# Kernel optimization log

Measured on AMD Instinct MI355X. Metric: run time of the kernel, lower is better.

## Reference

```python
import jax, jax.numpy as jnp
import numpy as np

DIM = 768
HEADS = 12
DIM_HEAD = DIM // HEADS
FACTOR = DIM_HEAD ** (-0.5)
B, T = 4, 2048


def setup_inputs() -> dict:
    key = jax.random.key(0)
    k1, k2, k3 = jax.random.split(key, 3)
    x = jax.random.normal(k1, (B, T, DIM), dtype=jnp.float32)
    # VarianceScaling-like init scale for linear weights
    W_qkv = jax.random.normal(k2, (DIM, 3 * DIM), dtype=jnp.float32) * (DIM ** -0.5)
    W_out = jax.random.normal(k3, (DIM, DIM), dtype=jnp.float32) * (DIM ** -0.5)
    return {"x": x, "W_qkv": W_qkv, "W_out": W_out}


def reference(x, W_qkv, W_out):
    b, t, _ = x.shape
    qkv = x @ W_qkv  # [b, t, 3*dim]
    # einops 'b t (d k h) -> k b h t d' with k=3, h=HEADS: d slowest, k middle, h fastest
    qkv = qkv.reshape(b, t, DIM_HEAD, 3, HEADS)
    qkv = jnp.transpose(qkv, (3, 0, 4, 1, 2))  # [3, b, h, t, d]
    q, k, v = qkv[0], qkv[1], qkv[2]
    # scaled dot-product attention, full [b,h,t,t] scores as in the original
    scores = jnp.einsum('bhid,bhjd->bhij', q, k) * FACTOR
    attn = jax.nn.softmax(scores, axis=-1)
    out = jnp.einsum('bhij,bhjd->bhid', attn, v)  # [b, h, t, d]
    # 'b h t d -> b t (h d)'
    out = jnp.transpose(out, (0, 2, 1, 3)).reshape(b, t, HEADS * DIM_HEAD)
    return out @ W_out
```

## Files before the change

kernel.cpp:

```cpp
#include <hip/hip_runtime.h>
#include <hip/hip_bf16.h>

#define DIM    768
#define HEADS  12
#define DHEAD  64
#define BATCH  4
#define SEQ    2048
#define NROW   (BATCH * SEQ)
#define QKVN   (3 * DIM)
#define FACTOR 0.125f

typedef __attribute__((ext_vector_type(8))) short short8;
typedef __attribute__((ext_vector_type(4))) float floatx4;

__device__ __forceinline__ floatx4 mfma16(short8 a, short8 b, floatx4 c) {
    return __builtin_amdgcn_mfma_f32_16x16x32_bf16(a, b, c, 0, 0, 0);
}

__device__ __forceinline__ short f2b(float f) {
    union { __hip_bfloat16 h; short s; } u;
    u.h = __float2bfloat16(f);
    return u.s;
}

__device__ __forceinline__ int swz8(int row, int col) {
    return (row << 6) + ((((col >> 3) ^ row) & 7) << 3) + (col & 7);
}

__global__ __launch_bounds__(256) void conv_bf16(const float* __restrict__ x,
                                                 short* __restrict__ xb) {
    int g = blockIdx.x * 256 + threadIdx.x;
    float4 v = ((const float4*)x)[g];
    uint2 o;
    o.x = (unsigned short)f2b(v.x) | ((unsigned)(unsigned short)f2b(v.y) << 16);
    o.y = (unsigned short)f2b(v.z) | ((unsigned)(unsigned short)f2b(v.w) << 16);
    ((uint2*)xb)[g] = o;
}

__global__ __launch_bounds__(256) void transpose_w(const float* __restrict__ W,
                                                   short* __restrict__ Wt,
                                                   int K, int N, int permute) {
    __shared__ short T[32][33];
    int n0 = blockIdx.x * 32, k0 = blockIdx.y * 32;
    int c = threadIdx.x & 31, r0 = threadIdx.x >> 5;
    for (int r = r0; r < 32; r += 8)
        T[r][c] = f2b(W[(size_t)(k0 + r) * N + n0 + c]);
    __syncthreads();
    for (int r = r0; r < 32; r += 8) {
        int n = n0 + r;
        int np;
        if (permute) {
            int d = n / 36, rem = n - d * 36;
            int which = rem / 12, h = rem - which * 12;
            np = which * 768 + h * 64 + d;
        } else {
            np = n;
        }
        Wt[(size_t)np * K + k0 + c] = T[c][r];
    }
}

__global__ __launch_bounds__(256) void gemm_qkv(const short* __restrict__ A,
                                                const short* __restrict__ Bt,
                                                short* __restrict__ Qo,
                                                short* __restrict__ Ko,
                                                short* __restrict__ Vto) {
    __shared__ short As[128 * 64];
    __shared__ short Bs[128 * 64];
    const int tid = threadIdx.x;
    const int lane = tid & 63, wave = tid >> 6;
    const int l15 = lane & 15, quad = lane >> 4;

    const int flat = blockIdx.x;
    const int xcd = flat & 7;
    const int local = flat >> 3;
    const int mloc = local & 7, nloc = local >> 3;
    const int m0 = (xcd * 8 + mloc) * 128;
    const int n0 = nloc * 128;

    const int wm = (wave >> 1) * 64, wn = (wave & 1) * 64;

    floatx4 acc[4][4] = {};
    for (int k0 = 0; k0 < DIM; k0 += 64) {
#pragma unroll
        for (int i = 0; i < 4; ++i) {
            int idx = tid + i * 256;
            int row = idx >> 3, c = idx & 7;
            int loff = (row << 6) + (((c ^ row) & 7) << 3);
            *(uint4*)&As[loff] = *(const uint4*)&A[(size_t)(m0 + row) * DIM + k0 + c * 8];
            *(uint4*)&Bs[loff] = *(const uint4*)&Bt[(size_t)(n0 + row) * DIM + k0 + c * 8];
        }
        __syncthreads();
#pragma unroll
        for (int ks = 0; ks < 2; ++ks) {
            short8 a[4], b[4];
#pragma unroll
            for (int mt = 0; mt < 4; ++mt)
                a[mt] = *(const short8*)&As[swz8(wm + mt * 16 + l15, ks * 32 + quad * 8)];
#pragma unroll
            for (int nt = 0; nt < 4; ++nt)
                b[nt] = *(const short8*)&Bs[swz8(wn + nt * 16 + l15, ks * 32 + quad * 8)];
#pragma unroll
            for (int mt = 0; mt < 4; ++mt)
#pragma unroll
                for (int nt = 0; nt < 4; ++nt)
                    acc[mt][nt] = mfma16(a[mt], b[nt], acc[mt][nt]);
        }
        __syncthreads();
    }

    const int sn = n0 + wn;
    const int which = sn / 768;
    const int h = (sn - which * 768) >> 6;
    const int bb = (m0 + wm) >> 11;
    const int tbase = (m0 + wm) & 2047;

    if (which != 2) {
        short* dst = (which == 0) ? Qo : Ko;
        const size_t rowbase = ((size_t)(bb * HEADS + h) * SEQ + tbase) * DHEAD;
#pragma unroll
        for (int mt = 0; mt < 4; ++mt)
#pragma unroll
            for (int nt = 0; nt < 4; ++nt) {
                int d = nt * 16 + l15;
#pragma unroll
                for (int r = 0; r < 4; ++r) {
                    int tl = mt * 16 + quad * 4 + r;
                    dst[rowbase + (size_t)tl * DHEAD + d] = f2b(acc[mt][nt][r]);
                }
            }
    } else {
        short* vld = ((wave < 2) ? As : Bs) + (wave & 1) * 4096;
#pragma unroll
        for (int mt = 0; mt < 4; ++mt)
#pragma unroll
            for (int nt = 0; nt < 4; ++nt) {
                int d = nt * 16 + l15;
                int tl = mt * 16 + quad * 4;
                int chunk = (tl >> 3) ^ (d & 7);
                int addr = (d << 6) + (chunk << 3) + (tl & 7);
                short4 pk;
                pk.x = f2b(acc[mt][nt][0]);
                pk.y = f2b(acc[mt][nt][1]);
                pk.z = f2b(acc[mt][nt][2]);
                pk.w = f2b(acc[mt][nt][3]);
                *(short4*)&vld[addr] = pk;
            }
    }
    __syncthreads();
    if (which == 2) {
        short* vld = ((wave < 2) ? As : Bs) + (wave & 1) * 4096;
        const size_t vbase = ((size_t)(bb * HEADS + h) * DHEAD) * SEQ;
#pragma unroll
        for (int i = 0; i < 8; ++i) {
            int c = lane + i * 64;
            int d = c >> 3, j = c & 7;
            int addr = (d << 6) + (((j ^ (d & 7)) & 7) << 3);
            uint4 v = *(const uint4*)&vld[addr];
            *(uint4*)&Vto[vbase + (size_t)d * SEQ + tbase + j * 8] = v;
        }
    }
}

__global__ __launch_bounds__(256) void attn_mfma(const short* __restrict__ Q,
                                                 const short* __restrict__ K,
                                                 const short* __restrict__ Vt,
                                                 short* __restrict__ O) {
    __shared__ short Qs[128 * 64];
    __shared__ short Ks[64 * 64];
    __shared__ short Vs[64 * 64];
    __shared__ short Ps[4 * 32 * 64];

    const int tid = threadIdx.x;
    const int lane = tid & 63, wave = tid >> 6;
    const int l15 = lane & 15, quad = lane >> 4;
    const int bh = blockIdx.y;
    const int q0 = blockIdx.x * 128;
    const size_t base = (size_t)bh * SEQ * DHEAD;
    const int wr = wave * 32;
    short* myP = Ps + wave * (32 * 64);
    const float LOG2E_F = 1.4426950408889634f * FACTOR;

#pragma unroll
    for (int i = 0; i < 4; ++i) {
        int idx = tid + i * 256;
        int row = idx >> 3, c = idx & 7;
        *(uint4*)&Qs[(row << 6) + (((c ^ row) & 7) << 3)] =
            *(const uint4*)&Q[base + (size_t)(q0 + row) * DHEAD + c * 8];
    }

    floatx4 o[2][4] = {};
    float lsum[2][4] = {};

    for (int j0 = 0; j0 < SEQ; j0 += 64) {
#pragma unroll
        for (int i = 0; i < 2; ++i) {
            int idx = tid + i * 256;
            int row = idx >> 3, c = idx & 7;
            int loff = (row << 6) + (((c ^ row) & 7) << 3);
            *(uint4*)&Ks[loff] = *(const uint4*)&K[base + (size_t)(j0 + row) * DHEAD + c * 8];
            *(uint4*)&Vs[loff] = *(const uint4*)&Vt[base + (size_t)row * SEQ + j0 + c * 8];
        }
        __syncthreads();

        floatx4 s[2][4] = {};
#pragma unroll
        for (int ks = 0; ks < 2; ++ks) {
            short8 a[2], b[4];
#pragma unroll
            for (int mt = 0; mt < 2; ++mt)
                a[mt] = *(const short8*)&Qs[swz8(wr + mt * 16 + l15, ks * 32 + quad * 8)];
#pragma unroll
            for (int nt = 0; nt < 4; ++nt)
                b[nt] = *(const short8*)&Ks[swz8(nt * 16 + l15, ks * 32 + quad * 8)];
#pragma unroll
            for (int mt = 0; mt < 2; ++mt)
#pragma unroll
                for (int nt = 0; nt < 4; ++nt)
                    s[mt][nt] = mfma16(a[mt], b[nt], s[mt][nt]);
        }

#pragma unroll
        for (int mt = 0; mt < 2; ++mt)
#pragma unroll
            for (int r = 0; r < 4; ++r) {
                int lrow = mt * 16 + quad * 4 + r;
                float rs = 0.f;
#pragma unroll
                for (int nt = 0; nt < 4; ++nt) {
                    float p = __builtin_amdgcn_exp2f(s[mt][nt][r] * LOG2E_F);
                    rs += p;
                    myP[swz8(lrow, nt * 16 + l15)] = f2b(p);
                }
                lsum[mt][r] += rs;
            }

#pragma unroll
        for (int ks = 0; ks < 2; ++ks) {
            short8 a[2], b[4];
#pragma unroll
            for (int mt = 0; mt < 2; ++mt)
                a[mt] = *(const short8*)&myP[swz8(mt * 16 + l15, ks * 32 + quad * 8)];
#pragma unroll
            for (int dt = 0; dt < 4; ++dt)
                b[dt] = *(const short8*)&Vs[swz8(dt * 16 + l15, ks * 32 + quad * 8)];
#pragma unroll
            for (int mt = 0; mt < 2; ++mt)
#pragma unroll
                for (int dt = 0; dt < 4; ++dt)
                    o[mt][dt] = mfma16(a[mt], b[dt], o[mt][dt]);
        }
        __syncthreads();
    }

    const int b = bh / HEADS, h = bh - b * HEADS;
#pragma unroll
    for (int mt = 0; mt < 2; ++mt)
#pragma unroll
        for (int r = 0; r < 4; ++r) {
            float rs = lsum[mt][r];
#pragma unroll
            for (int off = 1; off < 16; off <<= 1) rs += __shfl_xor(rs, off);
            float inv = 1.f / rs;
            int t = q0 + wr + mt * 16 + quad * 4 + r;
#pragma unroll
            for (int dt = 0; dt < 4; ++dt) {
                int d = dt * 16 + l15;
                O[((size_t)(b * SEQ + t)) * DIM + h * DHEAD + d] =
                    f2b(o[mt][dt][r] * inv);
            }
        }
}

__global__ __launch_bounds__(256) void gemm_out(const short* __restrict__ A,
                                                const short* __restrict__ Bt,
                                                float* __restrict__ out) {
    __shared__ short As[128 * 64];
    __shared__ short Bs[128 * 64];
    const int tid = threadIdx.x;
    const int lane = tid & 63, wave = tid >> 6;
    const int l15 = lane & 15, quad = lane >> 4;
    const int m0 = blockIdx.y * 128, n0 = blockIdx.x * 128;
    const int wm = (wave >> 1) * 64, wn = (wave & 1) * 64;

    floatx4 acc[4][4] = {};
    for (int k0 = 0; k0 < DIM; k0 += 64) {
#pragma unroll
        for (int i = 0; i < 4; ++i) {
            int idx = tid + i * 256;
            int row = idx >> 3, c = idx & 7;
            int loff = (row << 6) + (((c ^ row) & 7) << 3);
            *(uint4*)&As[loff] = *(const uint4*)&A[(size_t)(m0 + row) * DIM + k0 + c * 8];
            *(uint4*)&Bs[loff] = *(const uint4*)&Bt[(size_t)(n0 + row) * DIM + k0 + c * 8];
        }
        __syncthreads();
#pragma unroll
        for (int ks = 0; ks < 2; ++ks) {
            short8 a[4], b[4];
#pragma unroll
            for (int mt = 0; mt < 4; ++mt)
                a[mt] = *(const short8*)&As[swz8(wm + mt * 16 + l15, ks * 32 + quad * 8)];
#pragma unroll
            for (int nt = 0; nt < 4; ++nt)
                b[nt] = *(const short8*)&Bs[swz8(wn + nt * 16 + l15, ks * 32 + quad * 8)];
#pragma unroll
            for (int mt = 0; mt < 4; ++mt)
#pragma unroll
                for (int nt = 0; nt < 4; ++nt)
                    acc[mt][nt] = mfma16(a[mt], b[nt], acc[mt][nt]);
        }
        __syncthreads();
    }

#pragma unroll
    for (int mt = 0; mt < 4; ++mt)
#pragma unroll
        for (int nt = 0; nt < 4; ++nt)
#pragma unroll
            for (int r = 0; r < 4; ++r) {
                int m = m0 + wm + mt * 16 + quad * 4 + r;
                int n = n0 + wn + nt * 16 + l15;
                out[(size_t)m * DIM + n] = acc[mt][nt][r];
            }
}

extern "C" void kernel_launch(void* const* d_in, const int* in_sizes, int n_in,
                              void* d_out, int out_size, void* d_ws, size_t ws_size,
                              hipStream_t stream) {
    const float* x    = (const float*)d_in[0];
    const float* Wqkv = (const float*)d_in[1];
    const float* Wout = (const float*)d_in[2];
    float* out = (float*)d_out;

    const size_t NE = (size_t)NROW * DIM;
    short* xb  = (short*)d_ws;
    short* Wqt = xb + NE;
    short* Wot = Wqt + (size_t)QKVN * DIM;
    short* Qw  = Wot + (size_t)DIM * DIM;
    short* Kw  = Qw + NE;
    short* Vtw = Kw + NE;

    conv_bf16<<<NE / 4 / 256, 256, 0, stream>>>(x, xb);
    transpose_w<<<dim3(QKVN / 32, DIM / 32), 256, 0, stream>>>(Wqkv, Wqt, DIM, QKVN, 1);
    transpose_w<<<dim3(DIM / 32, DIM / 32), 256, 0, stream>>>(Wout, Wot, DIM, DIM, 0);
    gemm_qkv<<<8 * 8 * 18, 256, 0, stream>>>(xb, Wqt, Qw, Kw, Vtw);
    attn_mfma<<<dim3(SEQ / 128, BATCH * HEADS), 256, 0, stream>>>(Qw, Kw, Vtw, xb);
    gemm_out<<<dim3(DIM / 128, NROW / 128), 256, 0, stream>>>(xb, Wot, out);
}
```

Before: 253.9 us.

## Fold softmax scale into Q and compute transposed scores for packed P stores

Folds the softmax factor times log2(e) into Q when the QKV GEMM writes it out, so the attention loop applies exp2 directly without a per-element multiply. It also swaps the MFMA operands so each lane holds four consecutive keys of one query row, which lets P be packed two at a time into 64-bit LDS stores and the row sums be reduced with two shuffles instead of four. The generic bf16 conversion is replaced by a hand-written round-to-nearest-even bit trick with pairwise packing. Scaling Q before rounding to bf16 changes rounding slightly, and the no-max softmax still depends on the scores staying small.

```diff
diff --git a/kernel.cpp b/kernel.cpp
--- a/kernel.cpp
+++ b/kernel.cpp
@@ -9,6 +9,7 @@
 #define NROW   (BATCH * SEQ)
 #define QKVN   (3 * DIM)
 #define FACTOR 0.125f
+#define QSCALE 0.18033688011112042f
 
 typedef __attribute__((ext_vector_type(8))) short short8;
 typedef __attribute__((ext_vector_type(4))) float floatx4;
@@ -17,10 +18,16 @@
     return __builtin_amdgcn_mfma_f32_16x16x32_bf16(a, b, c, 0, 0, 0);
 }
 
-__device__ __forceinline__ short f2b(float f) {
-    union { __hip_bfloat16 h; short s; } u;
-    u.h = __float2bfloat16(f);
-    return u.s;
+__device__ __forceinline__ short rne16(float f) {
+    unsigned u = __builtin_bit_cast(unsigned, f);
+    return (short)((u + 0x7fffu + ((u >> 16) & 1u)) >> 16);
+}
+__device__ __forceinline__ unsigned pack2(float lo, float hi) {
+    unsigned ul = __builtin_bit_cast(unsigned, lo);
+    unsigned uh = __builtin_bit_cast(unsigned, hi);
+    ul = (ul + 0x7fffu + ((ul >> 16) & 1u)) >> 16;
+    uh = (uh + 0x7fffu + ((uh >> 16) & 1u)) & 0xffff0000u;
+    return ul | uh;
 }
 
 __device__ __forceinline__ int swz8(int row, int col) {
@@ -32,8 +39,8 @@
     int g = blockIdx.x * 256 + threadIdx.x;
     float4 v = ((const float4*)x)[g];
     uint2 o;
-    o.x = (unsigned short)f2b(v.x) | ((unsigned)(unsigned short)f2b(v.y) << 16);
-    o.y = (unsigned short)f2b(v.z) | ((unsigned)(unsigned short)f2b(v.w) << 16);
+    o.x = pack2(v.x, v.y);
+    o.y = pack2(v.z, v.w);
     ((uint2*)xb)[g] = o;
 }
 
@@ -44,7 +51,7 @@
     int n0 = blockIdx.x * 32, k0 = blockIdx.y * 32;
     int c = threadIdx.x & 31, r0 = threadIdx.x >> 5;
     for (int r = r0; r < 32; r += 8)
-        T[r][c] = f2b(W[(size_t)(k0 + r) * N + n0 + c]);
+        T[r][c] = rne16(W[(size_t)(k0 + r) * N + n0 + c]);
     __syncthreads();
     for (int r = r0; r < 32; r += 8) {
         int n = n0 + r;
@@ -117,6 +124,7 @@
 
     if (which != 2) {
         short* dst = (which == 0) ? Qo : Ko;
+        const float scale = (which == 0) ? QSCALE : 1.0f;
         const size_t rowbase = ((size_t)(bb * HEADS + h) * SEQ + tbase) * DHEAD;
 #pragma unroll
         for (int mt = 0; mt < 4; ++mt)
@@ -126,7 +134,7 @@
 #pragma unroll
                 for (int r = 0; r < 4; ++r) {
                     int tl = mt * 16 + quad * 4 + r;
-                    dst[rowbase + (size_t)tl * DHEAD + d] = f2b(acc[mt][nt][r]);
+                    dst[rowbase + (size_t)tl * DHEAD + d] = rne16(acc[mt][nt][r] * scale);
                 }
             }
     } else {
@@ -139,12 +147,10 @@
                 int tl = mt * 16 + quad * 4;
                 int chunk = (tl >> 3) ^ (d & 7);
                 int addr = (d << 6) + (chunk << 3) + (tl & 7);
-                short4 pk;
-                pk.x = f2b(acc[mt][nt][0]);
-                pk.y = f2b(acc[mt][nt][1]);
-                pk.z = f2b(acc[mt][nt][2]);
-                pk.w = f2b(acc[mt][nt][3]);
-                *(short4*)&vld[addr] = pk;
+                uint2 pk;
+                pk.x = pack2(acc[mt][nt][0], acc[mt][nt][1]);
+                pk.y = pack2(acc[mt][nt][2], acc[mt][nt][3]);
+                *(uint2*)&vld[addr] = pk;
             }
     }
     __syncthreads();
@@ -179,7 +185,6 @@
     const size_t base = (size_t)bh * SEQ * DHEAD;
     const int wr = wave * 32;
     short* myP = Ps + wave * (32 * 64);
-    const float LOG2E_F = 1.4426950408889634f * FACTOR;
 
 #pragma unroll
     for (int i = 0; i < 4; ++i) {
@@ -190,7 +195,7 @@
     }
 
     floatx4 o[2][4] = {};
-    float lsum[2][4] = {};
+    float lsum[2] = {0.f, 0.f};
 
     for (int j0 = 0; j0 < SEQ; j0 += 64) {
 #pragma unroll
@@ -206,33 +211,33 @@
         floatx4 s[2][4] = {};
 #pragma unroll
         for (int ks = 0; ks < 2; ++ks) {
-            short8 a[2], b[4];
+            short8 kf[4], qf[2];
+#pragma unroll
+            for (int kt = 0; kt < 4; ++kt)
+                kf[kt] = *(const short8*)&Ks[swz8(kt * 16 + l15, ks * 32 + quad * 8)];
 #pragma unroll
             for (int mt = 0; mt < 2; ++mt)
-                a[mt] = *(const short8*)&Qs[swz8(wr + mt * 16 + l15, ks * 32 + quad * 8)];
-#pragma unroll
-            for (int nt = 0; nt < 4; ++nt)
-                b[nt] = *(const short8*)&Ks[swz8(nt * 16 + l15, ks * 32 + quad * 8)];
+                qf[mt] = *(const short8*)&Qs[swz8(wr + mt * 16 + l15, ks * 32 + quad * 8)];
 #pragma unroll
             for (int mt = 0; mt < 2; ++mt)
 #pragma unroll
-                for (int nt = 0; nt < 4; ++nt)
-                    s[mt][nt] = mfma16(a[mt], b[nt], s[mt][nt]);
+                for (int kt = 0; kt < 4; ++kt)
+                    s[mt][kt] = mfma16(kf[kt], qf[mt], s[mt][kt]);
         }
 
 #pragma unroll
         for (int mt = 0; mt < 2; ++mt)
 #pragma unroll
-            for (int r = 0; r < 4; ++r) {
-                int lrow = mt * 16 + quad * 4 + r;
-                float rs = 0.f;
-#pragma unroll
-                for (int nt = 0; nt < 4; ++nt) {
-                    float p = __builtin_amdgcn_exp2f(s[mt][nt][r] * LOG2E_F);
-                    rs += p;
-                    myP[swz8(lrow, nt * 16 + l15)] = f2b(p);
-                }
-                lsum[mt][r] += rs;
+            for (int kt = 0; kt < 4; ++kt) {
+                float p0 = __builtin_amdgcn_exp2f(s[mt][kt][0]);
+                float p1 = __builtin_amdgcn_exp2f(s[mt][kt][1]);
+                float p2 = __builtin_amdgcn_exp2f(s[mt][kt][2]);
+                float p3 = __builtin_amdgcn_exp2f(s[mt][kt][3]);
+                lsum[mt] += (p0 + p1) + (p2 + p3);
+                uint2 pk;
+                pk.x = pack2(p0, p1);
+                pk.y = pack2(p2, p3);
+                *(uint2*)&myP[swz8(mt * 16 + l15, kt * 16 + quad * 4)] = pk;
             }
 
 #pragma unroll
@@ -255,21 +260,23 @@
 
     const int b = bh / HEADS, h = bh - b * HEADS;
 #pragma unroll
-    for (int mt = 0; mt < 2; ++mt)
+    for (int mt = 0; mt < 2; ++mt) {
+        float rs = lsum[mt];
+        rs += __shfl_xor(rs, 16);
+        rs += __shfl_xor(rs, 32);
+        float invl = 1.f / rs;
 #pragma unroll
         for (int r = 0; r < 4; ++r) {
-            float rs = lsum[mt][r];
-#pragma unroll
-            for (int off = 1; off < 16; off <<= 1) rs += __shfl_xor(rs, off);
-            float inv = 1.f / rs;
+            float inv = __shfl(invl, quad * 4 + r);
             int t = q0 + wr + mt * 16 + quad * 4 + r;
 #pragma unroll
             for (int dt = 0; dt < 4; ++dt) {
                 int d = dt * 16 + l15;
                 O[((size_t)(b * SEQ + t)) * DIM + h * DHEAD + d] =
-                    f2b(o[mt][dt][r] * inv);
-            }
-        }
+                    rne16(o[mt][dt][r] * inv);
+            }
+        }
+    }
 }
 
 __global__ __launch_bounds__(256) void gemm_out(const short* __restrict__ A,
```

Measured after the change: 253.4 us. Within noise of the previous version (-0.2%).
